# Performance work log

Hardware: AMD Instinct MI355X
Metric: run time of the kernel (lower is better)

The kernel has to match this reference:

```python
import jax, jax.numpy as jnp
import numpy as np

D_MODEL = 256
D_STATE = 16
D_CONV = 4
EXPAND = 2
D_INNER = EXPAND * D_MODEL  # 512
DT_RANK = 16  # ceil(256/16)
BATCH = 4
SEQLEN = 2048


def causal_dwconv(x, w, b):
    # x: (B, D, L), w: (D, 1, K) depthwise, causal left-pad K-1 (matches padding=K-1 then truncate to L)
    K = w.shape[-1]
    y = jax.lax.conv_general_dilated(
        x, w, window_strides=(1,), padding=[(K - 1, 0)],
        feature_group_count=x.shape[1], dimension_numbers=('NCH', 'OIH', 'NCH'))
    return y + b[None, :, None]


def selective_scan(u, delta, A, Bm, Cm, D, z):
    # u, delta, z: (B, Dn, L); A: (Dn, N); Bm, Cm: (B, N, L); D: (Dn,)
    dT = jnp.moveaxis(delta, -1, 0)   # (L, B, Dn)
    uT = jnp.moveaxis(u, -1, 0)       # (L, B, Dn)
    BT = jnp.moveaxis(Bm, -1, 0)      # (L, B, N)
    CT = jnp.moveaxis(Cm, -1, 0)      # (L, B, N)
    h0 = jnp.zeros((u.shape[0], u.shape[1], A.shape[1]), u.dtype)

    def step(h, xs):
        d, ut, bt, ct = xs
        dA = jnp.exp(d[..., None] * A)                       # (B, Dn, N)
        h = dA * h + (d * ut)[..., None] * bt[:, None, :]    # h_t = dA*h + delta*B*u
        y = jnp.einsum('bdn,bn->bd', h, ct)
        return h, y

    _, yT = jax.lax.scan(step, h0, (dT, uT, BT, CT))
    y = jnp.moveaxis(yT, 0, -1)                              # (B, Dn, L)
    return (y + u * D[:, None]) * jax.nn.silu(z)


def mamba_branch(xz, conv_w, conv_b, x_w, dt_w, dt_b, A, D):
    # xz: (B, 2*Dn, L)
    x, z = jnp.split(xz, 2, axis=1)
    x = jax.nn.silu(causal_dwconv(x, conv_w, conv_b))
    x_dbl = jnp.einsum('bdl,rd->brl', x, x_w)                # (B, R+2N, L)
    dt, Bm, Cm = jnp.split(x_dbl, [DT_RANK, DT_RANK + D_STATE], axis=1)
    delta = jax.nn.softplus(jnp.einsum('brl,dr->bdl', dt, dt_w) + dt_b[None, :, None])
    return selective_scan(x, delta, A, Bm, Cm, D, z)


def stream_forward(h, A, A_b, in_w, conv_w, conv_b, x_w, dt_w, dt_b, Dp,
                   conv_w_b, conv_b_b, x_w_b, dt_w_b, dt_b_b, Dp_b, out_w):
    # h: (B, L, Dm) -> xz: (B, 2*Dn, L); in_proj has no bias (bias=False)
    xz = jnp.einsum('bld,ed->bel', h, in_w)
    y_f = mamba_branch(xz, conv_w, conv_b, x_w, dt_w, dt_b, A, Dp)
    y_r = mamba_branch(jnp.flip(xz, -1), conv_w_b, conv_b_b, x_w_b, dt_w_b, dt_b_b, A_b, Dp_b)
    y = 0.5 * y_f + 0.5 * jnp.flip(y_r, -1)                  # if_devide_out=True
    return jnp.einsum('bdl,md->blm', y, out_w)               # out_proj, no bias


def reference(a_hidden_states, v_hidden_states, A_log, A_b_log,
              a_in_w, a_conv_w, a_conv_b, a_x_w, a_dt_w, a_dt_b, a_D,
              a_conv_w_b, a_conv_b_b, a_x_w_b, a_dt_w_b, a_dt_b_b, a_D_b, a_out_w,
              v_in_w, v_conv_w, v_conv_b, v_x_w, v_dt_w, v_dt_b, v_D,
              v_conv_w_b, v_conv_b_b, v_x_w_b, v_dt_w_b, v_dt_b_b, v_D_b, v_out_w):
    A = -jnp.exp(A_log)
    A_b = -jnp.exp(A_b_log)
    a_out = stream_forward(a_hidden_states, A, A_b, a_in_w, a_conv_w, a_conv_b, a_x_w,
                           a_dt_w, a_dt_b, a_D, a_conv_w_b, a_conv_b_b, a_x_w_b,
                           a_dt_w_b, a_dt_b_b, a_D_b, a_out_w)
    v_out = stream_forward(v_hidden_states, A, A_b, v_in_w, v_conv_w, v_conv_b, v_x_w,
                           v_dt_w, v_dt_b, v_D, v_conv_w_b, v_conv_b_b, v_x_w_b,
                           v_dt_w_b, v_dt_b_b, v_D_b, v_out_w)
    return (a_out, v_out)


def setup_inputs() -> dict:
    key = jax.random.key(0)
    ks = iter(jax.random.split(key, 64))

    def nrm(shape, s):
        return jax.random.normal(next(ks), shape, jnp.float32) * s

    def dt_bias():
        # inverse-softplus of dt sampled log-uniform in [1e-3, 1e-1], as in the torch init
        dt = jnp.exp(jax.random.uniform(next(ks), (D_INNER,)) * (np.log(0.1) - np.log(0.001)) + np.log(0.001))
        dt = jnp.clip(dt, 1e-4)
        return dt + jnp.log(-jnp.expm1(-dt))

    A_log = jnp.log(jnp.broadcast_to(jnp.arange(1, D_STATE + 1, dtype=jnp.float32), (D_INNER, D_STATE)))

    def stream_params():
        return dict(
            in_w=nrm((2 * D_INNER, D_MODEL), D_MODEL ** -0.5),
            conv_w=nrm((D_INNER, 1, D_CONV), D_CONV ** -0.5),
            conv_b=jnp.zeros((D_INNER,), jnp.float32),
            x_w=nrm((DT_RANK + 2 * D_STATE, D_INNER), D_INNER ** -0.5),
            dt_w=nrm((D_INNER, DT_RANK), DT_RANK ** -0.5),
            dt_b=dt_bias(),
            D=jnp.ones((D_INNER,), jnp.float32),
            conv_w_b=nrm((D_INNER, 1, D_CONV), D_CONV ** -0.5),
            conv_b_b=jnp.zeros((D_INNER,), jnp.float32),
            x_w_b=nrm((DT_RANK + 2 * D_STATE, D_INNER), D_INNER ** -0.5),
            dt_w_b=nrm((D_INNER, DT_RANK), DT_RANK ** -0.5),
            dt_b_b=dt_bias(),
            D_b=jnp.ones((D_INNER,), jnp.float32),
            out_w=nrm((D_MODEL, D_INNER), D_INNER ** -0.5),
        )

    a, v = stream_params(), stream_params()
    inp = {
        'a_hidden_states': jax.random.normal(next(ks), (BATCH, SEQLEN, D_MODEL), jnp.float32),
        'v_hidden_states': jax.random.normal(next(ks), (BATCH, SEQLEN, D_MODEL), jnp.float32),
        'A_log': A_log,
        'A_b_log': A_log,
    }
    for pfx, p in (('a_', a), ('v_', v)):
        for k, val in p.items():
            inp[pfx + k] = val
    return inp
```

## Files before the change

### kernel.cpp

```cpp
#include <hip/hip_runtime.h>
#include <hip/hip_bf16.h>
#include <cstddef>

#define BB 4
#define LL 2048
#define DM 256
#define DN 512
#define EE 1024
#define NS 16
#define RK 16
#define NC2 128
#define CL2 (LL / NC2)
#define NLT (LL / 16)
#define G2C (2 * BB * DN)
#define SZC ((size_t)BB * LL * DN)
#define NSZC ((size_t)BB * LL * NS)
#define HSZC ((size_t)NC2 * G2C * NS)
#define XWSL (48 * 512)

typedef __attribute__((ext_vector_type(8))) short bf16x8;
typedef __attribute__((ext_vector_type(8))) unsigned short ushort8;
typedef __attribute__((ext_vector_type(4))) unsigned short ushort4v;
typedef __attribute__((ext_vector_type(2))) unsigned short ushort2v;
typedef __attribute__((ext_vector_type(4))) float f32x4;
typedef __attribute__((ext_vector_type(2))) float f32x2;

__device__ __forceinline__ float fsilu(float x) { return x / (1.0f + __expf(-x)); }
__device__ __forceinline__ float fsoftplus_fast(float x) {
  return x > 20.0f ? x : __logf(1.0f + __expf(x));
}
__device__ __forceinline__ unsigned short f2bf(float x) {
  union { float f; unsigned int u; } v; v.f = x;
  unsigned int r = v.u + 0x7fffu + ((v.u >> 16) & 1u);
  return (unsigned short)(r >> 16);
}
__device__ __forceinline__ float bf2f(unsigned short x) {
  union { unsigned int u; float f; } v; v.u = ((unsigned int)x) << 16;
  return v.f;
}

__global__ __launch_bounds__(256) void in_proj_mfma(
    const float* __restrict__ h_a, const float* __restrict__ h_v,
    const float* __restrict__ w_a, const float* __restrict__ w_v,
    unsigned short* __restrict__ xz, unsigned short* __restrict__ z_t) {
  __shared__ unsigned short ht[64][40];
  __shared__ unsigned short wt[128][40];
  const int bz = blockIdx.z;
  const int b = bz & 3;
  const int str = bz >> 2;
  const float* h = str ? h_v : h_a;
  const float* w = str ? w_v : w_a;
  unsigned short* xzs = xz + (size_t)str * SZC;
  unsigned short* zts = z_t + (size_t)str * SZC;
  const int e0 = blockIdx.y * 128;
  const int l0 = blockIdx.x * 64;
  const int tid = threadIdx.x;
  const int lane = tid & 63;
  const int wv = tid >> 6;
  const bool zblk = (e0 >= DN);
  const int krow = (lane >> 4) * 8;
  const int rlo = lane & 15;
  const int rbase = (lane >> 4) * 4;

  f32x4 acc[8];
#pragma unroll
  for (int i = 0; i < 8; i++) acc[i] = (f32x4){0.f, 0.f, 0.f, 0.f};

  for (int dk = 0; dk < DM; dk += 32) {
    {
      int row = tid >> 2;
      int seg = (tid & 3) * 8;
      const float* hp = h + ((size_t)b * LL + l0 + row) * DM + dk + seg;
      float4 ha = *(const float4*)hp, hb = *(const float4*)(hp + 4);
      ushort8 hv;
      hv[0] = f2bf(ha.x); hv[1] = f2bf(ha.y); hv[2] = f2bf(ha.z); hv[3] = f2bf(ha.w);
      hv[4] = f2bf(hb.x); hv[5] = f2bf(hb.y); hv[6] = f2bf(hb.z); hv[7] = f2bf(hb.w);
      *(ushort8*)&ht[row][seg] = hv;
    }
#pragma unroll
    for (int it = 0; it < 2; it++) {
      int idx = it * 256 + tid;
      int row = idx >> 2;
      int seg = (idx & 3) * 8;
      const float* wp = w + (size_t)(e0 + row) * DM + dk + seg;
      float4 wa = *(const float4*)wp, wb = *(const float4*)(wp + 4);
      ushort8 wv8;
      wv8[0] = f2bf(wa.x); wv8[1] = f2bf(wa.y); wv8[2] = f2bf(wa.z); wv8[3] = f2bf(wa.w);
      wv8[4] = f2bf(wb.x); wv8[5] = f2bf(wb.y); wv8[6] = f2bf(wb.z); wv8[7] = f2bf(wb.w);
      *(ushort8*)&wt[row][seg] = wv8;
    }
    __syncthreads();
    if (!zblk) {
      bf16x8 af0 = *(bf16x8*)&wt[wv * 32 + 0 * 16 + rlo][krow];
      bf16x8 af1 = *(bf16x8*)&wt[wv * 32 + 1 * 16 + rlo][krow];
      bf16x8 bf0 = *(bf16x8*)&ht[0 * 16 + rlo][krow];
      bf16x8 bf1 = *(bf16x8*)&ht[1 * 16 + rlo][krow];
      bf16x8 bf2 = *(bf16x8*)&ht[2 * 16 + rlo][krow];
      bf16x8 bf3 = *(bf16x8*)&ht[3 * 16 + rlo][krow];
      acc[0] = __builtin_amdgcn_mfma_f32_16x16x32_bf16(af0, bf0, acc[0], 0, 0, 0);
      acc[1] = __builtin_amdgcn_mfma_f32_16x16x32_bf16(af0, bf1, acc[1], 0, 0, 0);
      acc[2] = __builtin_amdgcn_mfma_f32_16x16x32_bf16(af0, bf2, acc[2], 0, 0, 0);
      acc[3] = __builtin_amdgcn_mfma_f32_16x16x32_bf16(af0, bf3, acc[3], 0, 0, 0);
      acc[4] = __builtin_amdgcn_mfma_f32_16x16x32_bf16(af1, bf0, acc[4], 0, 0, 0);
      acc[5] = __builtin_amdgcn_mfma_f32_16x16x32_bf16(af1, bf1, acc[5], 0, 0, 0);
      acc[6] = __builtin_amdgcn_mfma_f32_16x16x32_bf16(af1, bf2, acc[6], 0, 0, 0);
      acc[7] = __builtin_amdgcn_mfma_f32_16x16x32_bf16(af1, bf3, acc[7], 0, 0, 0);
    } else {
      bf16x8 af0 = *(bf16x8*)&ht[0 * 16 + rlo][krow];
      bf16x8 af1 = *(bf16x8*)&ht[1 * 16 + rlo][krow];
      bf16x8 af2 = *(bf16x8*)&ht[2 * 16 + rlo][krow];
      bf16x8 af3 = *(bf16x8*)&ht[3 * 16 + rlo][krow];
      bf16x8 bf0 = *(bf16x8*)&wt[wv * 32 + 0 * 16 + rlo][krow];
      bf16x8 bf1 = *(bf16x8*)&wt[wv * 32 + 1 * 16 + rlo][krow];
      acc[0] = __builtin_amdgcn_mfma_f32_16x16x32_bf16(af0, bf0, acc[0], 0, 0, 0);
      acc[1] = __builtin_amdgcn_mfma_f32_16x16x32_bf16(af0, bf1, acc[1], 0, 0, 0);
      acc[2] = __builtin_amdgcn_mfma_f32_16x16x32_bf16(af1, bf0, acc[2], 0, 0, 0);
      acc[3] = __builtin_amdgcn_mfma_f32_16x16x32_bf16(af1, bf1, acc[3], 0, 0, 0);
      acc[4] = __builtin_amdgcn_mfma_f32_16x16x32_bf16(af2, bf0, acc[4], 0, 0, 0);
      acc[5] = __builtin_amdgcn_mfma_f32_16x16x32_bf16(af2, bf1, acc[5], 0, 0, 0);
      acc[6] = __builtin_amdgcn_mfma_f32_16x16x32_bf16(af3, bf0, acc[6], 0, 0, 0);
      acc[7] = __builtin_amdgcn_mfma_f32_16x16x32_bf16(af3, bf1, acc[7], 0, 0, 0);
    }
    __syncthreads();
  }
  if (!zblk) {
#pragma unroll
    for (int m = 0; m < 2; m++)
#pragma unroll
      for (int n = 0; n < 4; n++)
#pragma unroll
        for (int r = 0; r < 4; r++) {
          int e = e0 + wv * 32 + m * 16 + rbase + r;
          int l = l0 + n * 16 + rlo;
          xzs[((size_t)b * DN + e) * LL + l] = f2bf(acc[m * 4 + n][r]);
        }
  } else {
#pragma unroll
    for (int m = 0; m < 4; m++)
#pragma unroll
      for (int n = 0; n < 2; n++)
#pragma unroll
        for (int r = 0; r < 4; r++) {
          int l = l0 + m * 16 + rbase + r;
          int d = (e0 - DN) + wv * 32 + n * 16 + rlo;
          zts[((size_t)b * LL + l) * DN + d] = f2bf(fsilu(acc[m * 2 + n][r]));
        }
  }
}

__global__ __launch_bounds__(256) void conv_kernel(
    const unsigned short* __restrict__ xz,
    const float* __restrict__ cw_af, const float* __restrict__ cb_af,
    const float* __restrict__ cw_ar, const float* __restrict__ cb_ar,
    const float* __restrict__ cw_vf, const float* __restrict__ cb_vf,
    const float* __restrict__ cw_vr, const float* __restrict__ cb_vr,
    unsigned short* __restrict__ u) {
  __shared__ float xt[128][33];
  const int slab = blockIdx.z;
  const int rev = slab & 1;
  const int str = slab >> 1;
  const int b = blockIdx.y;
  const int dc0 = (blockIdx.x & 3) * 128;
  const int l0 = (blockIdx.x >> 2) * 32;
  const int tid = threadIdx.x;
  const int lc = tid & 31;
  const int dg = tid >> 5;
  const int l = l0 + lc;
  const float* conv_w = str ? (rev ? cw_vr : cw_vf) : (rev ? cw_ar : cw_af);
  const float* conv_b = str ? (rev ? cb_vr : cb_vf) : (rev ? cb_ar : cb_af);
  const unsigned short* xzs = xz + (size_t)str * SZC;
  unsigned short* u_out = u + (size_t)slab * SZC;

#pragma unroll
  for (int i = 0; i < 16; i++) {
    int dloc = dg * 16 + i;
    int dd = dc0 + dloc;
    const unsigned short* base = xzs + ((size_t)b * DN + dd) * LL;
    float4 cw4 = *(const float4*)(conv_w + dd * 4);
    float a0 = conv_b[dd];
    if (rev) {
      a0 = fmaf(cw4.w, bf2f(base[l]), a0);
      if (l + 1 < LL) a0 = fmaf(cw4.z, bf2f(base[l + 1]), a0);
      if (l + 2 < LL) a0 = fmaf(cw4.y, bf2f(base[l + 2]), a0);
      if (l + 3 < LL) a0 = fmaf(cw4.x, bf2f(base[l + 3]), a0);
    } else {
      a0 = fmaf(cw4.w, bf2f(base[l]), a0);
      if (l - 1 >= 0) a0 = fmaf(cw4.z, bf2f(base[l - 1]), a0);
      if (l - 2 >= 0) a0 = fmaf(cw4.y, bf2f(base[l - 2]), a0);
      if (l - 3 >= 0) a0 = fmaf(cw4.x, bf2f(base[l - 3]), a0);
    }
    xt[dloc][lc] = fsilu(a0);
  }
  __syncthreads();
#pragma unroll
  for (int j = 0; j < 8; j++) {
    int idx = j * 256 + tid;
    int d2 = idx & 63;
    int l2 = idx >> 6;
    ushort2v v;
    v[0] = f2bf(xt[2 * d2][l2]);
    v[1] = f2bf(xt[2 * d2 + 1][l2]);
    *(ushort2v*)&u_out[((size_t)b * LL + l0 + l2) * DN + dc0 + 2 * d2] = v;
  }
}

__global__ __launch_bounds__(256) void xw_prep_kernel(
    const float* __restrict__ a_f, const float* __restrict__ a_r,
    const float* __restrict__ v_f, const float* __restrict__ v_r,
    unsigned short* __restrict__ o) {
  int i = blockIdx.x * 256 + threadIdx.x;
  if (i < XWSL) {
    o[i] = f2bf(a_f[i]);
    o[i + XWSL] = f2bf(a_r[i]);
    o[i + 2 * XWSL] = f2bf(v_f[i]);
    o[i + 3 * XWSL] = f2bf(v_r[i]);
  }
}

__global__ __launch_bounds__(256) void xdbl_kernel(
    const unsigned short* __restrict__ u, const unsigned short* __restrict__ xwbf,
    float* __restrict__ dtv_g, float* __restrict__ Bb, float* __restrict__ Cb) {
  __shared__ __align__(16) unsigned short ub[4][16][136];
  __shared__ float red[4][48][17];
  const int slab = blockIdx.z;
  const int b = blockIdx.y;
  const int lt = blockIdx.x;
  const int l0 = lt * 16;
  const int tid = threadIdx.x;
  const int lane = tid & 63;
  const int w = tid >> 6;
  const int rlo = lane & 15;
  const int hi4 = lane >> 4;
  const int kseg = hi4 * 8;

  const unsigned short* up = u + (size_t)slab * SZC + ((size_t)b * LL + l0) * DN;
  const unsigned short* xwb = xwbf + (size_t)slab * XWSL;
  float* B_out = Bb + (size_t)slab * NSZC;
  float* C_out = Cb + (size_t)slab * NSZC;

#pragma unroll
  for (int j = 0; j < 4; j++) {
    int idx = j * 256 + tid;
    int l2 = idx >> 6;
    int c8 = idx & 63;
    ushort8 v = *(const ushort8*)(up + (size_t)l2 * DN + c8 * 8);
    *(ushort8*)&ub[c8 >> 4][l2][(c8 & 15) * 8] = v;
  }
  __syncthreads();

  f32x4 am0 = (f32x4){0.f, 0.f, 0.f, 0.f};
  f32x4 am1 = (f32x4){0.f, 0.f, 0.f, 0.f};
  f32x4 am2 = (f32x4){0.f, 0.f, 0.f, 0.f};
#pragma unroll
  for (int ks = 0; ks < 4; ks++) {
    bf16x8 bfrag = *(bf16x8*)&ub[w][rlo][ks * 32 + kseg];
    const unsigned short* xp = xwb + (size_t)(w * 128 + ks * 32 + kseg);
    bf16x8 a0 = *(const bf16x8*)(xp + (size_t)(0 + rlo) * 512);
    bf16x8 a1 = *(const bf16x8*)(xp + (size_t)(16 + rlo) * 512);
    bf16x8 a2 = *(const bf16x8*)(xp + (size_t)(32 + rlo) * 512);
    am0 = __builtin_amdgcn_mfma_f32_16x16x32_bf16(a0, bfrag, am0, 0, 0, 0);
    am1 = __builtin_amdgcn_mfma_f32_16x16x32_bf16(a1, bfrag, am1, 0, 0, 0);
    am2 = __builtin_amdgcn_mfma_f32_16x16x32_bf16(a2, bfrag, am2, 0, 0, 0);
  }
  {
    const int rbase = hi4 * 4;
#pragma unroll
    for (int r = 0; r < 4; r++) red[w][0 + rbase + r][rlo] = am0[r];
#pragma unroll
    for (int r = 0; r < 4; r++) red[w][16 + rbase + r][rlo] = am1[r];
#pragma unroll
    for (int r = 0; r < 4; r++) red[w][32 + rbase + r][rlo] = am2[r];
  }
  __syncthreads();
  float* dtvp = dtv_g + (((size_t)slab * BB + b) * NLT + lt) * 256;
#pragma unroll
  for (int i = 0; i < 3; i++) {
    int o = i * 256 + tid;
    int row = o >> 4, col = o & 15;
    float s = (red[0][row][col] + red[1][row][col]) +
              (red[2][row][col] + red[3][row][col]);
    if (row < 16)
      dtvp[(size_t)row * 16 + col] = s;
    else if (row < 32)
      B_out[((size_t)b * LL + l0 + col) * NS + (row - 16)] = s;
    else
      C_out[((size_t)b * LL + l0 + col) * NS + (row - 32)] = s;
  }
}

__global__ __launch_bounds__(256) void delta_kernel(
    const float* __restrict__ dtv_g,
    const float* __restrict__ dtw_af, const float* __restrict__ dtb_af,
    const float* __restrict__ dtw_ar, const float* __restrict__ dtb_ar,
    const float* __restrict__ dtw_vf, const float* __restrict__ dtb_vf,
    const float* __restrict__ dtw_vr, const float* __restrict__ dtb_vr,
    unsigned short* __restrict__ dl) {
  __shared__ __align__(16) float dtvT[16][20];
  const int slab = blockIdx.z;
  const int rev = slab & 1;
  const int str = slab >> 1;
  const int b = blockIdx.y;
  const int lt = blockIdx.x;
  const int l0 = lt * 16;
  const int tid = threadIdx.x;
  const float* dt_w = str ? (rev ? dtw_vr : dtw_vf) : (rev ? dtw_ar : dtw_af);
  const float* dt_b = str ? (rev ? dtb_vr : dtb_vf) : (rev ? dtb_ar : dtb_af);
  unsigned short* dl_out = dl + (size_t)slab * SZC;

  {
    const float* dtvp = dtv_g + (((size_t)slab * BB + b) * NLT + lt) * 256;
    float v = dtvp[tid];
    dtvT[tid & 15][tid >> 4] = v;
  }
  __syncthreads();

  const int dd0 = tid, dd1 = tid + 256;
  const float4* wr0 = (const float4*)(dt_w + (size_t)dd0 * RK);
  const float4* wr1 = (const float4*)(dt_w + (size_t)dd1 * RK);
  float4 a_0 = wr0[0], a_1 = wr0[1], a_2 = wr0[2], a_3 = wr0[3];
  float4 b_0 = wr1[0], b_1 = wr1[1], b_2 = wr1[2], b_3 = wr1[3];
  float bias0 = dt_b[dd0], bias1 = dt_b[dd1];

#pragma unroll
  for (int l2 = 0; l2 < 16; l2++) {
    float4 q0 = *(const float4*)&dtvT[l2][0];
    float4 q1 = *(const float4*)&dtvT[l2][4];
    float4 q2 = *(const float4*)&dtvT[l2][8];
    float4 q3 = *(const float4*)&dtvT[l2][12];
    float s0 = bias0, s1 = bias1;
    s0 = fmaf(a_0.x, q0.x, s0); s1 = fmaf(b_0.x, q0.x, s1);
    s0 = fmaf(a_0.y, q0.y, s0); s1 = fmaf(b_0.y, q0.y, s1);
    s0 = fmaf(a_0.z, q0.z, s0); s1 = fmaf(b_0.z, q0.z, s1);
    s0 = fmaf(a_0.w, q0.w, s0); s1 = fmaf(b_0.w, q0.w, s1);
    s0 = fmaf(a_1.x, q1.x, s0); s1 = fmaf(b_1.x, q1.x, s1);
    s0 = fmaf(a_1.y, q1.y, s0); s1 = fmaf(b_1.y, q1.y, s1);
    s0 = fmaf(a_1.z, q1.z, s0); s1 = fmaf(b_1.z, q1.z, s1);
    s0 = fmaf(a_1.w, q1.w, s0); s1 = fmaf(b_1.w, q1.w, s1);
    s0 = fmaf(a_2.x, q2.x, s0); s1 = fmaf(b_2.x, q2.x, s1);
    s0 = fmaf(a_2.y, q2.y, s0); s1 = fmaf(b_2.y, q2.y, s1);
    s0 = fmaf(a_2.z, q2.z, s0); s1 = fmaf(b_2.z, q2.z, s1);
    s0 = fmaf(a_2.w, q2.w, s0); s1 = fmaf(b_2.w, q2.w, s1);
    s0 = fmaf(a_3.x, q3.x, s0); s1 = fmaf(b_3.x, q3.x, s1);
    s0 = fmaf(a_3.y, q3.y, s0); s1 = fmaf(b_3.y, q3.y, s1);
    s0 = fmaf(a_3.z, q3.z, s0); s1 = fmaf(b_3.z, q3.z, s1);
    s0 = fmaf(a_3.w, q3.w, s0); s1 = fmaf(b_3.w, q3.w, s1);
    unsigned short* rowp = dl_out + ((size_t)b * LL + l0 + l2) * DN;
    rowp[dd0] = f2bf(fsoftplus_fast(s0));
    rowp[dd1] = f2bf(fsoftplus_fast(s1));
  }
}

template <int PHASE>
__global__ __launch_bounds__(256) void scan_kernel(
    unsigned short* __restrict__ u, const unsigned short* __restrict__ dl,
    const unsigned short* __restrict__ z_t, const float* __restrict__ Bb,
    const float* __restrict__ Cb, const float* __restrict__ A_log,
    const float* __restrict__ Ab_log,
    const float* __restrict__ D_af, const float* __restrict__ D_ar,
    const float* __restrict__ D_vf, const float* __restrict__ D_vr,
    unsigned short* __restrict__ hend, float* __restrict__ sumdl) {
  __shared__ unsigned short us[CL2][256];
  __shared__ unsigned short zs[CL2][256];
  __shared__ unsigned short dls[CL2][256];
  __shared__ __align__(16) float Bs[CL2][16];
  __shared__ __align__(16) float Cs[CL2][16];
  const int tid = threadIdx.x;
  const int str = blockIdx.y;
  const int ch0 = (blockIdx.x & 15) * 256;
  const int chunk = blockIdx.x >> 4;
  const int ch = ch0 + tid;
  const bool rev = ch0 >= BB * DN;
  const int slab = str * 2 + (rev ? 1 : 0);
  const int cid0 = rev ? ch0 - BB * DN : ch0;
  const int b = cid0 >> 9;
  const int d0 = cid0 & (DN - 1);
  const int d = d0 + tid;

  const float* Arow = (rev ? Ab_log : A_log) + d * NS;
  float Av[NS];
#pragma unroll
  for (int n = 0; n < NS; n++) Av[n] = -__expf(Arow[n]);
  bool fastA = true;
#pragma unroll
  for (int n = 0; n < NS; n++)
    if (fabsf(Av[n] + (float)(n + 1)) > 1e-4f * (float)(n + 1)) fastA = false;
  const float* Dsel = str ? (rev ? D_vr : D_vf) : (rev ? D_ar : D_af);
  const float Dd = Dsel[d];

  const int tlo = rev ? (LL - CL2 * (chunk + 1)) : (CL2 * chunk);
  unsigned short* uyb = u + (size_t)slab * SZC + ((size_t)b * LL + tlo) * DN + d0;
  const unsigned short* dlb = dl + (size_t)slab * SZC + ((size_t)b * LL + tlo) * DN + d0;
  const unsigned short* zb = z_t + (size_t)str * SZC + ((size_t)b * LL + tlo) * DN + d0;
  const float* Bp = Bb + (size_t)slab * NSZC + ((size_t)b * LL + tlo) * NS;
  const float* Cp = Cb + (size_t)slab * NSZC + ((size_t)b * LL + tlo) * NS;
  unsigned short* hendp = hend + (size_t)str * HSZC;
  float* sumdlp = sumdl + (size_t)str * NC2 * G2C;

  {
    const int lane = tid & 63;
    const int w = tid >> 6;
#pragma unroll
    for (int j4 = 0; j4 < 4; j4++) {
      int row = w * 4 + j4;
      ushort4v uu = *(const ushort4v*)(uyb + (size_t)row * DN + lane * 4);
      *(ushort4v*)&us[row][lane * 4] = uu;
      ushort4v dd4 = *(const ushort4v*)(dlb + (size_t)row * DN + lane * 4);
      *(ushort4v*)&dls[row][lane * 4] = dd4;
      if (PHASE == 3) {
        ushort4v zz = *(const ushort4v*)(zb + (size_t)row * DN + lane * 4);
        *(ushort4v*)&zs[row][lane * 4] = zz;
      }
    }
    Bs[tid >> 4][tid & 15] = Bp[(size_t)(tid >> 4) * NS + (tid & 15)];
    if (PHASE == 3) Cs[tid >> 4][tid & 15] = Cp[(size_t)(tid >> 4) * NS + (tid & 15)];
  }

  float h[NS];
  if (PHASE == 3) {
    const unsigned short* hp = hendp + ((size_t)chunk * G2C + ch) * NS;
#pragma unroll
    for (int n = 0; n < NS; n++) h[n] = bf2f(hp[n]);
  } else {
#pragma unroll
    for (int n = 0; n < NS; n++) h[n] = 0.f;
  }
  __syncthreads();

  float sdl = 0.f;
  if (fastA) {
    f32x2 h2[8];
#pragma unroll
    for (int k = 0; k < 8; k++) h2[k] = (f32x2){h[2 * k], h[2 * k + 1]};
#pragma unroll
    for (int jj = 0; jj < CL2; jj++) {
      const int j = rev ? (CL2 - 1 - jj) : jj;
      const float uc = bf2f(us[j][tid]);
      const float dc = bf2f(dls[j][tid]);
      const f32x2* B2 = (const f32x2*)&Bs[j][0];
      const f32x2* C2 = (const f32x2*)&Cs[j][0];
      const float dlu = dc * uc;
      const f32x2 dlu2 = (f32x2){dlu, dlu};
      const float p1 = __expf(-dc);
      const float p2 = p1 * p1;
      const f32x2 p22 = (f32x2){p2, p2};
      f32x2 P[8];
      P[0] = (f32x2){p1, p2};
#pragma unroll
      for (int k = 1; k < 8; k++) P[k] = P[k - 1] * p22;
      f32x2 acc2 = (f32x2){0.f, 0.f};
#pragma unroll
      for (int k = 0; k < 8; k++) {
        f32x2 db = dlu2 * B2[k];
        h2[k] = __builtin_elementwise_fma(P[k], h2[k], db);
        if (PHASE == 3) acc2 = __builtin_elementwise_fma(h2[k], C2[k], acc2);
      }
      if (PHASE == 1) sdl += dc;
      if (PHASE == 3) {
        const float zc = bf2f(zs[j][tid]);
        float y = fmaf(uc, Dd, acc2.x + acc2.y) * zc;
        uyb[(size_t)j * DN + tid] = f2bf(y);
      }
    }
#pragma unroll
    for (int k = 0; k < 8; k++) { h[2 * k] = h2[k].x; h[2 * k + 1] = h2[k].y; }
  } else {
#pragma unroll
    for (int jj = 0; jj < CL2; jj++) {
      const int j = rev ? (CL2 - 1 - jj) : jj;
      const float uc = bf2f(us[j][tid]);
      const float dc = bf2f(dls[j][tid]);
      const float dlu = dc * uc;
      float acc = 0.f;
#pragma unroll
      for (int n = 0; n < NS; n++) {
        h[n] = fmaf(__expf(dc * Av[n]), h[n], dlu * Bs[j][n]);
        if (PHASE == 3) acc = fmaf(h[n], Cs[j][n], acc);
      }
      if (PHASE == 1) sdl += dc;
      if (PHASE == 3) {
        const float zc = bf2f(zs[j][tid]);
        float y = fmaf(uc, Dd, acc) * zc;
        uyb[(size_t)j * DN + tid] = f2bf(y);
      }
    }
  }
  if (PHASE == 1) {
    unsigned short* hp = hendp + ((size_t)chunk * G2C + ch) * NS;
#pragma unroll
    for (int n = 0; n < NS; n++) hp[n] = f2bf(h[n]);
    sumdlp[(size_t)chunk * G2C + ch] = sdl;
  }
}

__global__ __launch_bounds__(256) void scan_combine_kernel(
    const float* __restrict__ A_log, const float* __restrict__ Ab_log,
    unsigned short* __restrict__ hend, const float* __restrict__ sumdl) {
  __shared__ float tile[8][256];
  __shared__ float sd[8][16];
  const int tid = threadIdx.x;
  const int str = blockIdx.y;
  const int ch0 = blockIdx.x * 16;
  const int chl = tid >> 4;
  const int n = tid & 15;
  const int ch = ch0 + chl;
  const bool rev = ch >= BB * DN;
  const int d = ch & (DN - 1);
  const float Av = -__expf((rev ? Ab_log : A_log)[d * NS + n]);
  unsigned short* hendp = hend + (size_t)str * HSZC;
  const float* sumdlp = sumdl + (size_t)str * NC2 * G2C;
  float H = 0.f;
  for (int cb = 0; cb < NC2 / 8; cb++) {
#pragma unroll
    for (int j = 0; j < 8; j++)
      tile[j][tid] = bf2f(hendp[((size_t)(cb * 8 + j) * G2C + ch0) * NS + tid]);
    if (tid < 128) {
      int j = tid >> 4, k = tid & 15;
      sd[j][k] = sumdlp[(size_t)(cb * 8 + j) * G2C + ch0 + k];
    }
    __syncthreads();
#pragma unroll
    for (int j = 0; j < 8; j++) {
      float tmp = tile[j][tid];
      tile[j][tid] = H;
      H = fmaf(__expf(Av * sd[j][chl]), H, tmp);
    }
    __syncthreads();
#pragma unroll
    for (int j = 0; j < 8; j++)
      hendp[((size_t)(cb * 8 + j) * G2C + ch0) * NS + tid] = f2bf(tile[j][tid]);
    __syncthreads();
  }
}

__global__ __launch_bounds__(256) void out_proj_mfma(
    const unsigned short* __restrict__ u,
    const float* __restrict__ ow_a, const float* __restrict__ ow_v,
    float* __restrict__ outp) {
  __shared__ unsigned short yt[64][40];
  __shared__ unsigned short wo[64][40];
  const int bz = blockIdx.z;
  const int b = bz & 3;
  const int str = bz >> 2;
  const float* ow = str ? ow_v : ow_a;
  const unsigned short* yf = u + (size_t)(str * 2) * SZC;
  const unsigned short* yr = u + (size_t)(str * 2 + 1) * SZC;
  float* outs = outp + (size_t)str * BB * LL * DM;
  const int m0 = blockIdx.y * 64;
  const int l0 = blockIdx.x * 64;
  const int tid = threadIdx.x;
  const int lane = tid & 63;
  const int wid = tid >> 6;
  const int wm = wid >> 1, wn = wid & 1;
  const int krow = (lane >> 4) * 8;
  const int rlo = lane & 15;

  f32x4 acc[2][2];
#pragma unroll
  for (int i = 0; i < 2; i++)
#pragma unroll
    for (int j = 0; j < 2; j++) acc[i][j] = (f32x4){0.f, 0.f, 0.f, 0.f};

  for (int dk = 0; dk < DN; dk += 32) {
    {
      int row = tid >> 2;
      int seg = (tid & 3) * 8;
      ushort8 a = *(const ushort8*)(yf + ((size_t)b * LL + l0 + row) * DN + dk + seg);
      ushort8 c = *(const ushort8*)(yr + ((size_t)b * LL + l0 + row) * DN + dk + seg);
      ushort8 yv;
#pragma unroll
      for (int k = 0; k < 8; k++) yv[k] = f2bf(0.5f * (bf2f(a[k]) + bf2f(c[k])));
      *(ushort8*)&yt[row][seg] = yv;
      const float* wp = ow + (size_t)(m0 + row) * DN + dk + seg;
      float4 w0 = *(const float4*)wp, w1 = *(const float4*)(wp + 4);
      ushort8 wv;
      wv[0] = f2bf(w0.x); wv[1] = f2bf(w0.y); wv[2] = f2bf(w0.z); wv[3] = f2bf(w0.w);
      wv[4] = f2bf(w1.x); wv[5] = f2bf(w1.y); wv[6] = f2bf(w1.z); wv[7] = f2bf(w1.w);
      *(ushort8*)&wo[row][seg] = wv;
    }
    __syncthreads();
    bf16x8 a0 = *(bf16x8*)&yt[wm * 32 + rlo][krow];
    bf16x8 a1 = *(bf16x8*)&yt[wm * 32 + 16 + rlo][krow];
    bf16x8 b0 = *(bf16x8*)&wo[wn * 32 + rlo][krow];
    bf16x8 b1 = *(bf16x8*)&wo[wn * 32 + 16 + rlo][krow];
    acc[0][0] = __builtin_amdgcn_mfma_f32_16x16x32_bf16(a0, b0, acc[0][0], 0, 0, 0);
    acc[0][1] = __builtin_amdgcn_mfma_f32_16x16x32_bf16(a0, b1, acc[0][1], 0, 0, 0);
    acc[1][0] = __builtin_amdgcn_mfma_f32_16x16x32_bf16(a1, b0, acc[1][0], 0, 0, 0);
    acc[1][1] = __builtin_amdgcn_mfma_f32_16x16x32_bf16(a1, b1, acc[1][1], 0, 0, 0);
    __syncthreads();
  }
#pragma unroll
  for (int mt = 0; mt < 2; mt++)
#pragma unroll
    for (int nt = 0; nt < 2; nt++)
#pragma unroll
      for (int r = 0; r < 4; r++) {
        int l = l0 + wm * 32 + mt * 16 + (lane >> 4) * 4 + r;
        int m = m0 + wn * 32 + nt * 16 + rlo;
        outs[((size_t)b * LL + l) * DM + m] = acc[mt][nt][r];
      }
}

extern "C" void kernel_launch(void* const* d_in, const int* in_sizes, int n_in,
                              void* d_out, int out_size, void* d_ws, size_t ws_size,
                              hipStream_t stream) {
  (void)in_sizes; (void)n_in; (void)out_size; (void)ws_size;
  const float* A_log = (const float*)d_in[2];
  const float* Ab_log = (const float*)d_in[3];
  const float* h_a = (const float*)d_in[0];
  const float* h_v = (const float*)d_in[1];
#define AP(i) ((const float*)d_in[4 + (i)])
#define VP(i) ((const float*)d_in[18 + (i)])

  float* ws = (float*)d_ws;
  float* Bb = ws;
  float* Cb = Bb + 4 * NSZC;
  float* sumdl = Cb + 4 * NSZC;
  float* dtv_g = sumdl + (size_t)2 * NC2 * G2C;
  unsigned short* xwbf = (unsigned short*)(dtv_g + (size_t)4 * BB * NLT * 256);
  unsigned short* z_t = xwbf + 4 * XWSL;
  unsigned short* u = z_t + 2 * SZC;
  unsigned short* xz = u + 4 * SZC;
  unsigned short* hend = xz + 2 * SZC;
  unsigned short* dl = hend + 2 * HSZC;

  hipLaunchKernelGGL(in_proj_mfma, dim3(LL / 64, EE / 128, BB * 2), dim3(256), 0,
                     stream, h_a, h_v, AP(0), VP(0), xz, z_t);
  hipLaunchKernelGGL(xw_prep_kernel, dim3(96), dim3(256), 0, stream,
                     AP(3), AP(9), VP(3), VP(9), xwbf);
  hipLaunchKernelGGL(conv_kernel, dim3((LL / 32) * 4, BB, 4), dim3(256), 0, stream,
                     xz, AP(1), AP(2), AP(7), AP(8), VP(1), VP(2), VP(7), VP(8), u);
  hipLaunchKernelGGL(xdbl_kernel, dim3(NLT, BB, 4), dim3(256), 0, stream,
                     u, xwbf, dtv_g, Bb, Cb);
  hipLaunchKernelGGL(delta_kernel, dim3(NLT, BB, 4), dim3(256), 0, stream,
                     dtv_g, AP(4), AP(5), AP(10), AP(11), VP(4), VP(5), VP(10),
                     VP(11), dl);
  hipLaunchKernelGGL(HIP_KERNEL_NAME(scan_kernel<1>), dim3(NC2 * 16, 2), dim3(256),
                     0, stream, u, dl, z_t, Bb, Cb, A_log, Ab_log, AP(6), AP(12),
                     VP(6), VP(12), hend, sumdl);
  hipLaunchKernelGGL(scan_combine_kernel, dim3(G2C / 16, 2), dim3(256), 0, stream,
                     A_log, Ab_log, hend, sumdl);
  hipLaunchKernelGGL(HIP_KERNEL_NAME(scan_kernel<3>), dim3(NC2 * 16, 2), dim3(256),
                     0, stream, u, dl, z_t, Bb, Cb, A_log, Ab_log, AP(6), AP(12),
                     VP(6), VP(12), hend, sumdl);
  hipLaunchKernelGGL(out_proj_mfma, dim3(LL / 64, DM / 64, BB * 2), dim3(256), 0,
                     stream, u, AP(13), VP(13), (float*)d_out);
#undef AP
#undef VP
}
```

Measured before the change: 220.9 us.

## Process multiple scan chunks per block with register-staged prefetch of next chunk

```diff
diff --git a/kernel.cpp b/kernel.cpp
--- a/kernel.cpp
+++ b/kernel.cpp
@@ -11,6 +11,7 @@
 #define RK 16
 #define NC2 128
 #define CL2 (LL / NC2)
+#define NCPB 4
 #define NLT (LL / 16)
 #define G2C (2 * BB * DN)
 #define SZC ((size_t)BB * LL * DN)
@@ -367,7 +368,7 @@
   const int tid = threadIdx.x;
   const int str = blockIdx.y;
   const int ch0 = (blockIdx.x & 15) * 256;
-  const int chunk = blockIdx.x >> 4;
+  const int cb0 = (blockIdx.x >> 4) * NCPB;
   const int ch = ch0 + tid;
   const bool rev = ch0 >= BB * DN;
   const int slab = str * 2 + (rev ? 1 : 0);
@@ -375,6 +376,8 @@
   const int b = cid0 >> 9;
   const int d0 = cid0 & (DN - 1);
   const int d = d0 + tid;
+  const int lane = tid & 63;
+  const int w = tid >> 6;
 
   const float* Arow = (rev ? Ab_log : A_log) + d * NS;
   float Av[NS];
@@ -387,108 +390,133 @@
   const float* Dsel = str ? (rev ? D_vr : D_vf) : (rev ? D_ar : D_af);
   const float Dd = Dsel[d];
 
-  const int tlo = rev ? (LL - CL2 * (chunk + 1)) : (CL2 * chunk);
-  unsigned short* uyb = u + (size_t)slab * SZC + ((size_t)b * LL + tlo) * DN + d0;
-  const unsigned short* dlb = dl + (size_t)slab * SZC + ((size_t)b * LL + tlo) * DN + d0;
-  const unsigned short* zb = z_t + (size_t)str * SZC + ((size_t)b * LL + tlo) * DN + d0;
-  const float* Bp = Bb + (size_t)slab * NSZC + ((size_t)b * LL + tlo) * NS;
-  const float* Cp = Cb + (size_t)slab * NSZC + ((size_t)b * LL + tlo) * NS;
+  unsigned short* ub_ = u + (size_t)slab * SZC + (size_t)b * LL * DN + d0;
+  const unsigned short* db_ = dl + (size_t)slab * SZC + (size_t)b * LL * DN + d0;
+  const unsigned short* zb_ = z_t + (size_t)str * SZC + (size_t)b * LL * DN + d0;
+  const float* Bp_ = Bb + (size_t)slab * NSZC + (size_t)b * LL * NS;
+  const float* Cp_ = Cb + (size_t)slab * NSZC + (size_t)b * LL * NS;
   unsigned short* hendp = hend + (size_t)str * HSZC;
   float* sumdlp = sumdl + (size_t)str * NC2 * G2C;
 
-  {
-    const int lane = tid & 63;
-    const int w = tid >> 6;
+  ushort4v ru[4], rd[4], rz[4];
+  float rB = 0.f, rC = 0.f;
+
+  auto stage_load = [&](int chunk) {
+    const int tlo = rev ? (LL - CL2 * (chunk + 1)) : (CL2 * chunk);
 #pragma unroll
     for (int j4 = 0; j4 < 4; j4++) {
       int row = w * 4 + j4;
-      ushort4v uu = *(const ushort4v*)(uyb + (size_t)row * DN + lane * 4);
-      *(ushort4v*)&us[row][lane * 4] = uu;
-      ushort4v dd4 = *(const ushort4v*)(dlb + (size_t)row * DN + lane * 4);
-      *(ushort4v*)&dls[row][lane * 4] = dd4;
-      if (PHASE == 3) {
-        ushort4v zz = *(const ushort4v*)(zb + (size_t)row * DN + lane * 4);
-        *(ushort4v*)&zs[row][lane * 4] = zz;
+      ru[j4] = *(const ushort4v*)(ub_ + ((size_t)(tlo + row)) * DN + lane * 4);
+      rd[j4] = *(const ushort4v*)(db_ + ((size_t)(tlo + row)) * DN + lane * 4);
+      if (PHASE == 3)
+        rz[j4] = *(const ushort4v*)(zb_ + ((size_t)(tlo + row)) * DN + lane * 4);
+    }
+    rB = Bp_[((size_t)(tlo + (tid >> 4))) * NS + (tid & 15)];
+    if (PHASE == 3) rC = Cp_[((size_t)(tlo + (tid >> 4))) * NS + (tid & 15)];
+  };
+  auto stage_write = [&]() {
+#pragma unroll
+    for (int j4 = 0; j4 < 4; j4++) {
+      int row = w * 4 + j4;
+      *(ushort4v*)&us[row][lane * 4] = ru[j4];
+      *(ushort4v*)&dls[row][lane * 4] = rd[j4];
+      if (PHASE == 3) *(ushort4v*)&zs[row][lane * 4] = rz[j4];
+    }
+    Bs[tid >> 4][tid & 15] = rB;
+    if (PHASE == 3) Cs[tid >> 4][tid & 15] = rC;
+  };
+
+  stage_load(cb0);
+  stage_write();
+  __syncthreads();
+
+  for (int i = 0; i < NCPB; i++) {
+    const int chunk = cb0 + i;
+    if (i + 1 < NCPB) stage_load(chunk + 1);
+
+    const int tlo = rev ? (LL - CL2 * (chunk + 1)) : (CL2 * chunk);
+    unsigned short* uyb = ub_ + (size_t)tlo * DN;
+
+    float h[NS];
+    if (PHASE == 3) {
+      const unsigned short* hp = hendp + ((size_t)chunk * G2C + ch) * NS;
+#pragma unroll
+      for (int n = 0; n < NS; n++) h[n] = bf2f(hp[n]);
+    } else {
+#pragma unroll
+      for (int n = 0; n < NS; n++) h[n] = 0.f;
+    }
+
+    float sdl = 0.f;
+    if (fastA) {
+      f32x2 h2[8];
+#pragma unroll
+      for (int k = 0; k < 8; k++) h2[k] = (f32x2){h[2 * k], h[2 * k + 1]};
+#pragma unroll
+      for (int jj = 0; jj < CL2; jj++) {
+        const int j = rev ? (CL2 - 1 - jj) : jj;
+        const float uc = bf2f(us[j][tid]);
+        const float dc = bf2f(dls[j][tid]);
+        const f32x2* B2 = (const f32x2*)&Bs[j][0];
+        const f32x2* C2 = (const f32x2*)&Cs[j][0];
+        const float dlu = dc * uc;
+        const f32x2 dlu2 = (f32x2){dlu, dlu};
+        const float p1 = __expf(-dc);
+        const float p2 = p1 * p1;
+        const f32x2 p22 = (f32x2){p2, p2};
+        f32x2 P[8];
+        P[0] = (f32x2){p1, p2};
+#pragma unroll
+        for (int k = 1; k < 8; k++) P[k] = P[k - 1] * p22;
+        f32x2 acc2 = (f32x2){0.f, 0.f};
+#pragma unroll
+        for (int k = 0; k < 8; k++) {
+          f32x2 db2 = dlu2 * B2[k];
+          h2[k] = __builtin_elementwise_fma(P[k], h2[k], db2);
+          if (PHASE == 3) acc2 = __builtin_elementwise_fma(h2[k], C2[k], acc2);
+        }
+        if (PHASE == 1) sdl += dc;
+        if (PHASE == 3) {
+          const float zc = bf2f(zs[j][tid]);
+          float y = fmaf(uc, Dd, acc2.x + acc2.y) * zc;
+          uyb[(size_t)j * DN + tid] = f2bf(y);
+        }
       }
-    }
-    Bs[tid >> 4][tid & 15] = Bp[(size_t)(tid >> 4) * NS + (tid & 15)];
-    if (PHASE == 3) Cs[tid >> 4][tid & 15] = Cp[(size_t)(tid >> 4) * NS + (tid & 15)];
-  }
-
-  float h[NS];
-  if (PHASE == 3) {
-    const unsigned short* hp = hendp + ((size_t)chunk * G2C + ch) * NS;
-#pragma unroll
-    for (int n = 0; n < NS; n++) h[n] = bf2f(hp[n]);
-  } else {
-#pragma unroll
-    for (int n = 0; n < NS; n++) h[n] = 0.f;
-  }
-  __syncthreads();
-
-  float sdl = 0.f;
-  if (fastA) {
-    f32x2 h2[8];
-#pragma unroll
-    for (int k = 0; k < 8; k++) h2[k] = (f32x2){h[2 * k], h[2 * k + 1]};
-#pragma unroll
-    for (int jj = 0; jj < CL2; jj++) {
-      const int j = rev ? (CL2 - 1 - jj) : jj;
-      const float uc = bf2f(us[j][tid]);
-      const float dc = bf2f(dls[j][tid]);
-      const f32x2* B2 = (const f32x2*)&Bs[j][0];
-      const f32x2* C2 = (const f32x2*)&Cs[j][0];
-      const float dlu = dc * uc;
-      const f32x2 dlu2 = (f32x2){dlu, dlu};
-      const float p1 = __expf(-dc);
-      const float p2 = p1 * p1;
-      const f32x2 p22 = (f32x2){p2, p2};
-      f32x2 P[8];
-      P[0] = (f32x2){p1, p2};
-#pragma unroll
-      for (int k = 1; k < 8; k++) P[k] = P[k - 1] * p22;
-      f32x2 acc2 = (f32x2){0.f, 0.f};
-#pragma unroll
-      for (int k = 0; k < 8; k++) {
-        f32x2 db = dlu2 * B2[k];
-        h2[k] = __builtin_elementwise_fma(P[k], h2[k], db);
-        if (PHASE == 3) acc2 = __builtin_elementwise_fma(h2[k], C2[k], acc2);
+#pragma unroll
+      for (int k = 0; k < 8; k++) { h[2 * k] = h2[k].x; h[2 * k + 1] = h2[k].y; }
+    } else {
+#pragma unroll
+      for (int jj = 0; jj < CL2; jj++) {
+        const int j = rev ? (CL2 - 1 - jj) : jj;
+        const float uc = bf2f(us[j][tid]);
+        const float dc = bf2f(dls[j][tid]);
+        const float dlu = dc * uc;
+        float acc = 0.f;
+#pragma unroll
+        for (int n = 0; n < NS; n++) {
+          h[n] = fmaf(__expf(dc * Av[n]), h[n], dlu * Bs[j][n]);
+          if (PHASE == 3) acc = fmaf(h[n], Cs[j][n], acc);
+        }
+        if (PHASE == 1) sdl += dc;
+        if (PHASE == 3) {
+          const float zc = bf2f(zs[j][tid]);
+          float y = fmaf(uc, Dd, acc) * zc;
+          uyb[(size_t)j * DN + tid] = f2bf(y);
+        }
       }
-      if (PHASE == 1) sdl += dc;
-      if (PHASE == 3) {
-        const float zc = bf2f(zs[j][tid]);
-        float y = fmaf(uc, Dd, acc2.x + acc2.y) * zc;
-        uyb[(size_t)j * DN + tid] = f2bf(y);
-      }
-    }
-#pragma unroll
-    for (int k = 0; k < 8; k++) { h[2 * k] = h2[k].x; h[2 * k + 1] = h2[k].y; }
-  } else {
-#pragma unroll
-    for (int jj = 0; jj < CL2; jj++) {
-      const int j = rev ? (CL2 - 1 - jj) : jj;
-      const float uc = bf2f(us[j][tid]);
-      const float dc = bf2f(dls[j][tid]);
-      const float dlu = dc * uc;
-      float acc = 0.f;
-#pragma unroll
-      for (int n = 0; n < NS; n++) {
-        h[n] = fmaf(__expf(dc * Av[n]), h[n], dlu * Bs[j][n]);
-        if (PHASE == 3) acc = fmaf(h[n], Cs[j][n], acc);
-      }
-      if (PHASE == 1) sdl += dc;
-      if (PHASE == 3) {
-        const float zc = bf2f(zs[j][tid]);
-        float y = fmaf(uc, Dd, acc) * zc;
-        uyb[(size_t)j * DN + tid] = f2bf(y);
-      }
-    }
-  }
-  if (PHASE == 1) {
-    unsigned short* hp = hendp + ((size_t)chunk * G2C + ch) * NS;
-#pragma unroll
-    for (int n = 0; n < NS; n++) hp[n] = f2bf(h[n]);
-    sumdlp[(size_t)chunk * G2C + ch] = sdl;
+    }
+    if (PHASE == 1) {
+      unsigned short* hp = hendp + ((size_t)chunk * G2C + ch) * NS;
+#pragma unroll
+      for (int n = 0; n < NS; n++) hp[n] = f2bf(h[n]);
+      sumdlp[(size_t)chunk * G2C + ch] = sdl;
+    }
+
+    if (i + 1 < NCPB) {
+      __syncthreads();
+      stage_write();
+      __syncthreads();
+    }
   }
 }
 
@@ -634,14 +662,14 @@
   hipLaunchKernelGGL(delta_kernel, dim3(NLT, BB, 4), dim3(256), 0, stream,
                      dtv_g, AP(4), AP(5), AP(10), AP(11), VP(4), VP(5), VP(10),
                      VP(11), dl);
-  hipLaunchKernelGGL(HIP_KERNEL_NAME(scan_kernel<1>), dim3(NC2 * 16, 2), dim3(256),
-                     0, stream, u, dl, z_t, Bb, Cb, A_log, Ab_log, AP(6), AP(12),
-                     VP(6), VP(12), hend, sumdl);
+  hipLaunchKernelGGL(HIP_KERNEL_NAME(scan_kernel<1>), dim3(NC2 / NCPB * 16, 2),
+                     dim3(256), 0, stream, u, dl, z_t, Bb, Cb, A_log, Ab_log,
+                     AP(6), AP(12), VP(6), VP(12), hend, sumdl);
   hipLaunchKernelGGL(scan_combine_kernel, dim3(G2C / 16, 2), dim3(256), 0, stream,
                      A_log, Ab_log, hend, sumdl);
-  hipLaunchKernelGGL(HIP_KERNEL_NAME(scan_kernel<3>), dim3(NC2 * 16, 2), dim3(256),
-                     0, stream, u, dl, z_t, Bb, Cb, A_log, Ab_log, AP(6), AP(12),
-                     VP(6), VP(12), hend, sumdl);
+  hipLaunchKernelGGL(HIP_KERNEL_NAME(scan_kernel<3>), dim3(NC2 / NCPB * 16, 2),
+                     dim3(256), 0, stream, u, dl, z_t, Bb, Cb, A_log, Ab_log,
+                     AP(6), AP(12), VP(6), VP(12), hend, sumdl);
   hipLaunchKernelGGL(out_proj_mfma, dim3(LL / 64, DM / 64, BB * 2), dim3(256), 0,
                      stream, u, AP(13), VP(13), (float*)d_out);
 #undef AP
```

Result: slower. 227.3 us (+2.9%).
